# Optimization experiments

Measured on AMD Instinct MI355X. Metric: run time of the kernel, lower is better.

## Reference

```python
import jax, jax.numpy as jnp
import numpy as np

CONF_THR = 0.3   # cfg.THRESHOLD_PREDICT_CONF
NMS_THR = 0.5    # cfg.THRESHOLD_PREDICT_NMS
TOPK = 500       # hard-coded topk(500) in forward


def _build_grid():
    # YOLOv3 @416: scales 13/26/52, 3 anchors each -> 10647 rows
    sizes = [13, 26, 52]
    anc = np.array([[10, 13], [16, 30], [33, 23], [30, 61], [62, 45], [59, 119],
                    [116, 90], [156, 198], [373, 326]], np.float32) / 416.0
    groups = [anc[6:9], anc[3:6], anc[0:3]]  # large anchors on coarse grid
    grids, anchors, fs = [], [], []
    for s, g in zip(sizes, groups):
        ys, xs = np.meshgrid(np.arange(s), np.arange(s), indexing='ij')
        gxy = np.stack([xs, ys], -1).astype(np.float32)          # [s,s,2]
        gxy = np.repeat(gxy.reshape(-1, 1, 2), 3, axis=1).reshape(-1, 2)
        grids.append(gxy)
        anchors.append(np.tile(g[None], (s * s, 1, 1)).reshape(-1, 2))
        fs.append(np.full((s * s * 3, 1), float(s), np.float32))
    return (np.concatenate(grids).astype(np.float32),
            np.concatenate(anchors).astype(np.float32),
            np.concatenate(fs).astype(np.float32))


def setup_inputs() -> dict:
    key = jax.random.key(0)
    k1, k2, k3 = jax.random.split(key, 3)
    B, A, C = 64, 10647, 80
    g, aw, fs = _build_grid()
    return {
        "pconf": jax.random.normal(k1, (B, A, 1), jnp.float32),
        "pcls": jax.random.normal(k2, (B, A, C), jnp.float32),
        "ptxywh": jax.random.normal(k3, (B, A, 4), jnp.float32),
        "grid_xy": jnp.asarray(g),
        "anchor_wh": jnp.asarray(aw),
        "fsize": jnp.asarray(fs),
    }


def _decode(ptxywh, grid_xy, anchor_wh, fsize):
    # boxes_decode4yolo3: sigmoid xy offset + cell, exp wh * anchor (all normalized)
    xy = (jax.nn.sigmoid(ptxywh[..., :2]) + grid_xy) / fsize   # [B,A,2]
    wh = jnp.exp(ptxywh[..., 2:]) * anchor_wh                  # [B,A,2]
    return jnp.concatenate([xy - 0.5 * wh, xy + 0.5 * wh], -1)  # ltrb


def _pairwise_iou(b):  # b: [K,4] ltrb
    area = jnp.maximum(b[:, 2] - b[:, 0], 0.) * jnp.maximum(b[:, 3] - b[:, 1], 0.)
    lt = jnp.maximum(b[:, None, :2], b[None, :, :2])
    rb = jnp.minimum(b[:, None, 2:], b[None, :, 2:])
    wh = jnp.maximum(rb - lt, 0.)
    inter = wh[..., 0] * wh[..., 1]
    return inter / (area[:, None] + area[None, :] - inter + 1e-9)


def _label_nms(boxes, labels, valid, thr):
    # boxes are pre-sorted by descending score (lax.top_k output order)
    K = boxes.shape[0]
    sup = (_pairwise_iou(boxes) > thr) & (labels[:, None] == labels[None, :])
    idx = jnp.arange(K)

    def body(suppressed, i):
        keep_i = valid[i] & ~suppressed[i]
        suppressed = suppressed | (keep_i & sup[i] & (idx > i))
        return suppressed, keep_i

    _, keep = jax.lax.scan(body, jnp.zeros(K, bool), idx)
    return keep


def reference(pconf, pcls, ptxywh, grid_xy, anchor_wh, fsize):
    B, A, _ = ptxywh.shape
    conf = jax.nn.sigmoid(pconf)[..., 0]            # [B,A]
    pc = jax.nn.sigmoid(pcls)                       # [B,A,C]
    cls_conf = pc.max(-1)
    plabels = pc.argmax(-1)
    pscores = cls_conf * conf                       # [B,A]

    vals, idx = jax.lax.top_k(pscores, TOPK)        # sorted desc, [B,K]
    valid = vals > CONF_THR                         # mask_pos AND mask_topk

    pltrb = _decode(ptxywh, grid_xy, anchor_wh, fsize)          # [B,A,4]
    boxes = jnp.take_along_axis(pltrb, idx[..., None], axis=1)  # [B,K,4]
    boxes = jnp.clip(boxes, 0.0, 1.0)
    labels = jnp.take_along_axis(plabels, idx, axis=1) + 1      # 1-based

    keep = jax.vmap(_label_nms, in_axes=(0, 0, 0, None))(boxes, labels, valid, NMS_THR)
    ids_batch = jnp.broadcast_to(jnp.arange(B)[:, None], (B, TOPK))
    return ids_batch, boxes, labels, vals, keep
```

## Files before the change

kernel.cpp:

```cpp
#include <hip/hip_runtime.h>
#include <math.h>

#define A_N 10647
#define C_N 80
#define K_N 500
#define CONF_THRF 0.3f
#define NMS_THRF 0.5f

#define NBUCK 1024
#define CAND_N 2048

#define SC_BLOCKS 2048

typedef float f32x4 __attribute__((ext_vector_type(4)));

__device__ __forceinline__ float sigmoid_ref(float x) {
    float e = expf(-x);
    return 1.0f / (1.0f + e);
}

__device__ __forceinline__ unsigned long long shfl_u64(unsigned long long v, int src) {
    unsigned int lo = (unsigned int)v, hi = (unsigned int)(v >> 32);
    lo = __shfl(lo, src, 64);
    hi = __shfl(hi, src, 64);
    return ((unsigned long long)hi << 32) | (unsigned long long)lo;
}

__device__ __forceinline__ unsigned long long shfl_xor_u64(unsigned long long v, int mask) {
    unsigned int lo = (unsigned int)v, hi = (unsigned int)(v >> 32);
    lo = __shfl_xor(lo, mask, 64);
    hi = __shfl_xor(hi, mask, 64);
    return ((unsigned long long)hi << 32) | (unsigned long long)lo;
}

__device__ __forceinline__ void reduce_row(
    const f32x4 v[5], int sub, float pc, size_t row,
    float* __restrict__ scores, int* __restrict__ labels) {
    float m = -3.4e38f;
    #pragma unroll
    for (int j = 0; j < 5; ++j)
        m = fmaxf(m, fmaxf(fmaxf(v[j][0], v[j][1]), fmaxf(v[j][2], v[j][3])));
    m = fmaxf(m, __shfl_xor(m, 1, 64));
    m = fmaxf(m, __shfl_xor(m, 2, 64));

    const float win = m - 1e-4f;
    int imin = 0x7FFFFFFF, cnt = 0;
    #pragma unroll
    for (int j = 0; j < 5; ++j) {
        #pragma unroll
        for (int t = 0; t < 4; ++t) {
            int idx = (sub + 4 * j) * 4 + t;
            if (v[j][t] == m && idx < imin) imin = idx;
            cnt += (v[j][t] >= win) ? 1 : 0;
        }
    }
    {
        int o = __shfl_xor(imin, 1, 64); imin = imin < o ? imin : o;
        o = __shfl_xor(imin, 2, 64);     imin = imin < o ? imin : o;
        cnt += __shfl_xor(cnt, 1, 64);
        cnt += __shfl_xor(cnt, 2, 64);
    }

    float sbest; int ibest;
    if (cnt >= 2) {
        unsigned long long key = 0ull;
        #pragma unroll
        for (int j = 0; j < 5; ++j) {
            #pragma unroll
            for (int t = 0; t < 4; ++t) {
                float x = v[j][t];
                if (x >= win) {
                    int idx = (sub + 4 * j) * 4 + t;
                    float s = sigmoid_ref(x);
                    unsigned long long k =
                        ((unsigned long long)__float_as_uint(s) << 32) |
                        (unsigned long long)(0xFFFFu - (unsigned)idx);
                    if (k > key) key = k;
                }
            }
        }
        unsigned long long o = shfl_xor_u64(key, 1); if (o > key) key = o;
        o = shfl_xor_u64(key, 2);                    if (o > key) key = o;
        sbest = __uint_as_float((unsigned int)(key >> 32));
        ibest = 0xFFFF - (int)(key & 0xFFFFull);
    } else {
        sbest = sigmoid_ref(m);
        ibest = imin;
    }

    if (sub == 0) {
        float cf = sigmoid_ref(pc);
        scores[row] = __fmul_rn(sbest, cf);
        labels[row] = ibest;
    }
}

__global__ __launch_bounds__(256) void score_kernel(
    const float* __restrict__ pconf,
    const float* __restrict__ pcls,
    float* __restrict__ scores,
    int* __restrict__ labels,
    int ntiles) {
    __shared__ float lds[4][1280];
    const int tid  = threadIdx.x;
    const int lane = tid & 63;
    const int wv   = tid >> 6;
    const int sub  = lane & 3;
    const int g    = lane >> 2;
    float* myl = lds[wv];

    int tile = blockIdx.x * 4 + wv;
    const int tstride = SC_BLOCKS * 4;
    if (tile >= ntiles) return;

    f32x4 v[5]; float pc;
    {
        const f32x4* tp = (const f32x4*)(pcls + (size_t)tile * 1280);
        #pragma unroll
        for (int j = 0; j < 5; ++j) v[j] = tp[j * 64 + lane];
        pc = pconf[tile * 16 + g];
    }

    while (true) {
        const int tnext = tile + tstride;
        const bool hasn = tnext < ntiles;
        f32x4 v2[5]; float pc2 = 0.0f;
        if (hasn) {
            const f32x4* tp = (const f32x4*)(pcls + (size_t)tnext * 1280);
            #pragma unroll
            for (int j = 0; j < 5; ++j) v2[j] = tp[j * 64 + lane];
            pc2 = pconf[tnext * 16 + g];
        }

        #pragma unroll
        for (int j = 0; j < 5; ++j)
            *(f32x4*)(myl + j * 256 + lane * 4) = v[j];
        f32x4 r[5];
        #pragma unroll
        for (int j = 0; j < 5; ++j)
            r[j] = *(const f32x4*)(myl + g * 80 + (sub + 4 * j) * 4);

        reduce_row(r, sub, pc, (size_t)tile * 16 + g, scores, labels);

        if (!hasn) break;
        #pragma unroll
        for (int j = 0; j < 5; ++j) v[j] = v2[j];
        pc = pc2;
        tile = tnext;
    }
}

__global__ __launch_bounds__(1024) void topk_nms_kernel(
    const float* __restrict__ scores,
    const int* __restrict__ labels,
    const float* __restrict__ ptxywh,
    const float* __restrict__ grid_xy,
    const float* __restrict__ anchor_wh,
    const float* __restrict__ fsize,
    float* __restrict__ out, int B) {
    extern __shared__ unsigned char smem[];
    unsigned int* hist = (unsigned int*)smem;
    unsigned long long* cand = (unsigned long long*)(smem + 4096);
    unsigned int* cntp = (unsigned int*)(smem + 20480);
    unsigned int* Tp   = (unsigned int*)(smem + 20484);
    const int b = blockIdx.x;
    const int tid = threadIdx.x;
    const float* sb = scores + (size_t)b * A_N;

    hist[tid] = 0u;
    cand[tid] = 0ull;
    cand[tid + 1024] = 0ull;
    if (tid == 0) *cntp = 0u;
    __syncthreads();

    for (int i = tid; i < A_N; i += 1024) {
        unsigned int u = __float_as_uint(sb[i]) >> 20;
        atomicAdd(&hist[u], 1u);
    }
    __syncthreads();

    for (int d = 1; d < NBUCK; d <<= 1) {
        unsigned int v = (tid + d < NBUCK) ? hist[tid + d] : 0u;
        __syncthreads();
        hist[tid] += v;
        __syncthreads();
    }
    if (hist[tid] >= K_N && (tid == NBUCK - 1 || hist[tid + 1] < K_N)) *Tp = (unsigned)tid;
    __syncthreads();
    const unsigned int T = *Tp;
    __syncthreads();

    for (int i = tid; i < A_N; i += 1024) {
        unsigned int u = __float_as_uint(sb[i]);
        if ((u >> 20) >= T) {
            unsigned int slot = atomicAdd(cntp, 1u);
            if (slot < CAND_N)
                cand[slot] = ((unsigned long long)u << 32) |
                             (unsigned long long)(0xFFFFu - (unsigned)i);
        }
    }
    __syncthreads();

    for (int sz = 2; sz <= CAND_N; sz <<= 1) {
        for (int j = sz >> 1; j > 0; j >>= 1) {
            int i = ((tid & ~(j - 1)) << 1) | (tid & (j - 1));
            int l = i | j;
            unsigned long long a = cand[i];
            unsigned long long c = cand[l];
            bool descBlk = ((i & sz) == 0);
            if (descBlk ? (a < c) : (a > c)) { cand[i] = c; cand[l] = a; }
            __syncthreads();
        }
    }

    unsigned long long myk = 0ull;
    if (tid < K_N) myk = cand[tid];
    __syncthreads();

    float* bxL   = (float*)smem;
    float* areaL = (float*)(smem + 8000);
    int*   labL  = (int*)  (smem + 10000);
    float* valsL = (float*)(smem + 12000);
    unsigned long long* nzL   = (unsigned long long*)(smem + 14016);
    unsigned long long* keepL = (unsigned long long*)(smem + 14080);
    unsigned long long* supL  = (unsigned long long*)(smem + 14336);

    if (tid >= 512 && tid < 520) nzL[tid - 512] = 0ull;

    const size_t BK = (size_t)B * K_N;
    if (tid < K_N) {
        float scv = __uint_as_float((unsigned int)(myk >> 32));
        int idx = 0xFFFF - (int)(myk & 0xFFFFull);
        int lb = labels[(size_t)b * A_N + idx] + 1;
        const float* t4 = ptxywh + ((size_t)b * A_N + idx) * 4;
        float tx = t4[0], ty = t4[1], tw = t4[2], th = t4[3];
        float gx = grid_xy[idx * 2 + 0], gy = grid_xy[idx * 2 + 1];
        float aw = anchor_wh[idx * 2 + 0], ah = anchor_wh[idx * 2 + 1];
        float fs = fsize[idx];
        float cx = __fdiv_rn(__fadd_rn(sigmoid_ref(tx), gx), fs);
        float cy = __fdiv_rn(__fadd_rn(sigmoid_ref(ty), gy), fs);
        float wx = __fmul_rn(expf(tw), aw);
        float wy = __fmul_rn(expf(th), ah);
        float hx = __fmul_rn(0.5f, wx);
        float hy = __fmul_rn(0.5f, wy);
        float x0 = __fsub_rn(cx, hx), y0 = __fsub_rn(cy, hy);
        float x1 = __fadd_rn(cx, hx), y1 = __fadd_rn(cy, hy);
        x0 = fminf(fmaxf(x0, 0.0f), 1.0f);
        y0 = fminf(fmaxf(y0, 0.0f), 1.0f);
        x1 = fminf(fmaxf(x1, 0.0f), 1.0f);
        y1 = fminf(fmaxf(y1, 0.0f), 1.0f);
        float area = __fmul_rn(fmaxf(__fsub_rn(x1, x0), 0.0f),
                               fmaxf(__fsub_rn(y1, y0), 0.0f));
        bxL[tid * 4 + 0] = x0; bxL[tid * 4 + 1] = y0;
        bxL[tid * 4 + 2] = x1; bxL[tid * 4 + 3] = y1;
        areaL[tid] = area; labL[tid] = lb; valsL[tid] = scv;

        out[(size_t)b * K_N + tid] = (float)b;
        float* ob = out + BK + ((size_t)b * K_N + tid) * 4;
        ob[0] = x0; ob[1] = y0; ob[2] = x1; ob[3] = y1;
        out[5 * BK + (size_t)b * K_N + tid] = (float)lb;
        out[6 * BK + (size_t)b * K_N + tid] = scv;
    }
    __syncthreads();

    for (int task = tid; task < K_N * 8; task += 1024) {
        int i = task >> 3;
        int w = task & 7;
        float li = bxL[i * 4 + 0], ti = bxL[i * 4 + 1];
        float ri = bxL[i * 4 + 2], bi = bxL[i * 4 + 3];
        float ai = areaL[i];
        int lbi = labL[i];
        unsigned long long bits = 0ull;
        int j0 = w * 64;
        int jend = j0 + 64; if (jend > K_N) jend = K_N;
        int jst = j0 > i + 1 ? j0 : i + 1;
        for (int j = jst; j < jend; ++j) {
            if (labL[j] == lbi) {
                float lj = bxL[j * 4 + 0], tj = bxL[j * 4 + 1];
                float rj = bxL[j * 4 + 2], bj = bxL[j * 4 + 3];
                float ltx = fmaxf(li, lj), lty = fmaxf(ti, tj);
                float rbx = fminf(ri, rj), rby = fminf(bi, bj);
                float iw = fmaxf(__fsub_rn(rbx, ltx), 0.0f);
                float ih = fmaxf(__fsub_rn(rby, lty), 0.0f);
                float inter = __fmul_rn(iw, ih);
                float den = __fadd_rn(__fsub_rn(__fadd_rn(ai, areaL[j]), inter), 1e-9f);
                float iou = __fdiv_rn(inter, den);
                if (iou > NMS_THRF) bits |= (1ull << (j - j0));
            }
        }
        supL[i * 8 + w] = bits;
        if (bits) atomicOr(&nzL[i >> 6], 1ull << (i & 63));
    }
    __syncthreads();

    if (tid < 64) {
        const int lane = tid;
        unsigned long long supp = 0ull, keepm = 0ull;
        unsigned long long nzreg = (lane < 8) ? nzL[lane] : 0ull;
        #pragma unroll
        for (int t = 0; t < 8; ++t) {
            const int i0 = t * 64;
            int myi = i0 + lane;
            bool v = (myi < K_N) ? (valsL[myi] > CONF_THRF) : false;
            unsigned long long vword = __ballot(v);
            unsigned long long nzword = shfl_u64(nzreg, t);
            const int imax = (K_N - i0 < 64) ? (K_N - i0) : 64;
            for (int i2 = 0; i2 < imax; ++i2) {
                unsigned long long sw = shfl_u64(supp, t);
                bool keep_i = ((vword >> i2) & 1ull) && !((sw >> i2) & 1ull);
                if (keep_i) {
                    if (lane == t) keepm |= (1ull << i2);
                    if ((nzword >> i2) & 1ull) {
                        if (lane < 8) supp |= supL[(i0 + i2) * 8 + lane];
                    }
                }
            }
        }
        if (lane < 8) keepL[lane] = keepm;
    }
    __syncthreads();

    if (tid < K_N) {
        unsigned long long kw = keepL[tid >> 6];
        out[7 * BK + (size_t)b * K_N + tid] = (float)((kw >> (tid & 63)) & 1ull);
    }
}

extern "C" void kernel_launch(void* const* d_in, const int* in_sizes, int n_in,
                              void* d_out, int out_size, void* d_ws, size_t ws_size,
                              hipStream_t stream) {
    const float* pconf     = (const float*)d_in[0];
    const float* pcls      = (const float*)d_in[1];
    const float* ptxywh    = (const float*)d_in[2];
    const float* grid_xy   = (const float*)d_in[3];
    const float* anchor_wh = (const float*)d_in[4];
    const float* fsize     = (const float*)d_in[5];
    int total = in_sizes[0];
    int B = total / A_N;
    if (B <= 0) return;
    int ntiles = total / 16;

    float* scores = (float*)d_ws;
    int*   labls  = (int*)((char*)d_ws + (size_t)total * sizeof(float));
    float* out    = (float*)d_out;

    hipLaunchKernelGGL(score_kernel, dim3(SC_BLOCKS), dim3(256), 0, stream,
                       pconf, pcls, scores, labls, ntiles);
    hipLaunchKernelGGL(topk_nms_kernel, dim3(B), dim3(1024), 46592, stream,
                       scores, labls, ptxywh, grid_xy, anchor_wh, fsize, out, B);
}
```

Measured before the change: 143.9 us.

## Stream score-kernel class tiles into LDS with double-buffered direct global-to-LDS loads

The score kernel now loads each block's 64-row tile of class logits straight into a double-buffered LDS array with global_load_lds. Before, each wave loaded its 16-row tile into registers and then copied it into LDS itself. Hand-placed vmcnt waits let the next tile's loads overlap the current tile's reduction. Block count is halved and launch bounds now request 4 blocks per CU. The goal is to cut register staging and LDS store traffic in this bandwidth-bound pass. The trade-off is reliance on fragile manual waitcnt accounting, and the tile count assumes the row total is a multiple of 64.

```diff
diff --git a/kernel.cpp b/kernel.cpp
--- a/kernel.cpp
+++ b/kernel.cpp
@@ -10,9 +10,17 @@
 #define NBUCK 1024
 #define CAND_N 2048
 
-#define SC_BLOCKS 2048
+#define SC_BLOCKS 1024
+#define TILE_ROWS 64
+#define TILE_FLOATS 5120
 
 typedef float f32x4 __attribute__((ext_vector_type(4)));
+
+__device__ __forceinline__ void gload_lds16(const float* g, float* l) {
+    __builtin_amdgcn_global_load_lds(
+        (__attribute__((address_space(1))) void*)const_cast<float*>(g),
+        (__attribute__((address_space(3))) void*)l, 16, 0, 0);
+}
 
 __device__ __forceinline__ float sigmoid_ref(float x) {
     float e = expf(-x);
@@ -95,58 +103,61 @@
     }
 }
 
-__global__ __launch_bounds__(256) void score_kernel(
+__global__ __launch_bounds__(256, 4) void score_kernel(
     const float* __restrict__ pconf,
     const float* __restrict__ pcls,
     float* __restrict__ scores,
     int* __restrict__ labels,
     int ntiles) {
-    __shared__ float lds[4][1280];
+    __shared__ float sbuf[2][TILE_FLOATS];
     const int tid  = threadIdx.x;
     const int lane = tid & 63;
     const int wv   = tid >> 6;
     const int sub  = lane & 3;
     const int g    = lane >> 2;
-    float* myl = lds[wv];
-
-    int tile = blockIdx.x * 4 + wv;
-    const int tstride = SC_BLOCKS * 4;
-    if (tile >= ntiles) return;
-
-    f32x4 v[5]; float pc;
+
+    const int tile0 = blockIdx.x;
+    const int tstride = SC_BLOCKS;
+    if (tile0 >= ntiles) return;
+
     {
-        const f32x4* tp = (const f32x4*)(pcls + (size_t)tile * 1280);
-        #pragma unroll
-        for (int j = 0; j < 5; ++j) v[j] = tp[j * 64 + lane];
-        pc = pconf[tile * 16 + g];
-    }
-
+        const float* src = pcls + (size_t)tile0 * TILE_FLOATS + wv * 1280 + lane * 4;
+        float* dst = &sbuf[0][wv * 1280];
+        #pragma unroll
+        for (int j = 0; j < 5; ++j) gload_lds16(src + j * 256, dst + j * 256);
+    }
+    float pc = pconf[(size_t)tile0 * TILE_ROWS + wv * 16 + g];
+
+    int tile = tile0;
+    int buf = 0;
     while (true) {
-        const int tnext = tile + tstride;
-        const bool hasn = tnext < ntiles;
-        f32x4 v2[5]; float pc2 = 0.0f;
+        const int tn = tile + tstride;
+        const bool hasn = tn < ntiles;
+        float pcn = 0.0f;
         if (hasn) {
-            const f32x4* tp = (const f32x4*)(pcls + (size_t)tnext * 1280);
+            const float* src = pcls + (size_t)tn * TILE_FLOATS + wv * 1280 + lane * 4;
+            float* dst = &sbuf[buf ^ 1][wv * 1280];
             #pragma unroll
-            for (int j = 0; j < 5; ++j) v2[j] = tp[j * 64 + lane];
-            pc2 = pconf[tnext * 16 + g];
-        }
-
+            for (int j = 0; j < 5; ++j) gload_lds16(src + j * 256, dst + j * 256);
+            pcn = pconf[(size_t)tn * TILE_ROWS + wv * 16 + g];
+            asm volatile("s_waitcnt vmcnt(7)" ::: "memory");
+        } else {
+            asm volatile("s_waitcnt vmcnt(0)" ::: "memory");
+        }
+        __builtin_amdgcn_sched_barrier(0);
+
+        const float* rowp = &sbuf[buf][(wv * 16 + g) * 80];
+        f32x4 r[5];
         #pragma unroll
         for (int j = 0; j < 5; ++j)
-            *(f32x4*)(myl + j * 256 + lane * 4) = v[j];
-        f32x4 r[5];
-        #pragma unroll
-        for (int j = 0; j < 5; ++j)
-            r[j] = *(const f32x4*)(myl + g * 80 + (sub + 4 * j) * 4);
-
-        reduce_row(r, sub, pc, (size_t)tile * 16 + g, scores, labels);
+            r[j] = *(const f32x4*)(rowp + (sub + 4 * j) * 4);
+
+        reduce_row(r, sub, pc, (size_t)tile * TILE_ROWS + wv * 16 + g, scores, labels);
 
         if (!hasn) break;
-        #pragma unroll
-        for (int j = 0; j < 5; ++j) v[j] = v2[j];
-        pc = pc2;
-        tile = tnext;
+        pc = pcn;
+        tile = tn;
+        buf ^= 1;
     }
 }
 
@@ -338,7 +349,7 @@
     int total = in_sizes[0];
     int B = total / A_N;
     if (B <= 0) return;
-    int ntiles = total / 16;
+    int ntiles = total / TILE_ROWS;
 
     float* scores = (float*)d_ws;
     int*   labls  = (int*)((char*)d_ws + (size_t)total * sizeof(float));
```

Result: no change. 144.0 us (+0.1%).
